# Kernel tuning notes

Hardware: AMD Instinct MI355X
Metric: run time of the kernel (lower is better)

Reference implementation:

```python
import jax, jax.numpy as jnp
import numpy as np

N = 50000      # nodes
E = 800000     # edges (avg degree 16)
D = 128        # input_nf = output_nf
H = 128        # hidden_nf


def _lin_init(key, fan_in, fan_out, gain=1.0):
    return gain * jax.random.normal(key, (fan_in, fan_out), jnp.float32) / np.sqrt(fan_in)


def setup_inputs() -> dict:
    key = jax.random.key(0)
    ks = jax.random.split(key, 20)
    h = jax.random.normal(ks[0], (N, D), jnp.float32)
    coord_diff = 0.5 * jax.random.normal(ks[1], (E, 3), jnp.float32)
    row = jax.random.randint(ks[2], (E,), 0, N, jnp.int32)
    col = jax.random.randint(ks[3], (E,), 0, N, jnp.int32)
    return {
        "h": h, "coord_diff": coord_diff, "row": row, "col": col,
        # edge_nn: Linear(2D+1 -> H), SiLU, Linear(H -> H), SiLU
        "We1": _lin_init(ks[4], 2 * D + 1, H), "be1": jnp.zeros((H,), jnp.float32),
        "We2": _lin_init(ks[5], H, H),          "be2": jnp.zeros((H,), jnp.float32),
        # node_nn: Linear(H+D -> H), SiLU, Linear(H -> D)
        "Wn1": _lin_init(ks[6], H + D, H), "bn1": jnp.zeros((H,), jnp.float32),
        "Wn2": _lin_init(ks[7], H, D),     "bn2": jnp.zeros((D,), jnp.float32),
        # coord_nn: Linear(H -> H), SiLU, Linear(H -> 1, no bias, gain 0.001)
        "Wc1": _lin_init(ks[8], H, H), "bc1": jnp.zeros((H,), jnp.float32),
        "Wc2": _lin_init(ks[9], H, 1, gain=0.001),
        # vel_scaling_nn: Linear(D -> H), SiLU, Linear(H -> 1)
        "Wv1": _lin_init(ks[10], D, H), "bv1": jnp.zeros((H,), jnp.float32),
        "Wv2": _lin_init(ks[11], H, 1), "bv2": jnp.zeros((1,), jnp.float32),
    }


def reference(h, coord_diff, row, col,
              We1, be1, We2, be2,
              Wn1, bn1, Wn2, bn2,
              Wc1, bc1, Wc2,
              Wv1, bv1, Wv2, bv2):
    n = h.shape[0]
    silu = jax.nn.silu
    # radial: squared edge length, [E,1]
    radial = jnp.sum(coord_diff * coord_diff, axis=1, keepdims=True)
    # edge model: gather endpoint features + radial, 2-layer SiLU MLP
    e_in = jnp.concatenate([h[row], h[col], radial], axis=1)        # [E, 2D+1]
    m = silu(silu(e_in @ We1 + be1) @ We2 + be2)                    # [E, H]
    # force model: per-edge scalar coefficient, clamped scatter-mean (coords_weight=1.0)
    coef = silu(m @ Wc1 + bc1) @ Wc2                                # [E, 1]
    trans = jnp.clip(coord_diff * coef, -100.0, 100.0)              # [E, 3]
    f_sum = jax.ops.segment_sum(trans, row, num_segments=n)         # [N, 3]
    cnt = jax.ops.segment_sum(jnp.ones((trans.shape[0], 1), trans.dtype), row, num_segments=n)
    force = f_sum / jnp.clip(cnt, 1.0)                              # segment mean, count clamped >=1
    # node model: scatter-sum of edge messages, then 2-layer MLP
    agg = jax.ops.segment_sum(m, row, num_segments=n)               # [N, H]
    h_cat = jnp.concatenate([h, agg], axis=1)                       # [N, D+H]
    h_out = silu(h_cat @ Wn1 + bn1) @ Wn2 + bn2                     # [N, D]
    # velocity scaling head
    vel = silu(h @ Wv1 + bv1) @ Wv2 + bv2                           # [N, 1]
    return (vel, force, h_out)
```

## Files before the change

### kernel.cpp

```cpp
#include <hip/hip_runtime.h>

#define NN 50000
#define EE 800000

typedef unsigned short u16;
typedef unsigned int u32;
typedef __attribute__((ext_vector_type(8))) short short8;
typedef __attribute__((ext_vector_type(4))) float f32x4;
typedef __attribute__((ext_vector_type(2))) float f32x2;

__device__ __forceinline__ u16 f2bf(float f) {
    union { float f; u32 i; } v; v.f = f;
    u32 x = v.i;
    return (u16)((x + 0x7fffu + ((x >> 16) & 1u)) >> 16);
}
__device__ __forceinline__ u32 pkr(float lo, float hi) {
    union { float f; u32 i; } a, b; a.f = lo; b.f = hi;
    return __builtin_amdgcn_perm(b.i + 0x8000u, a.i + 0x8000u, 0x07060302u);
}
__device__ __forceinline__ float bf2f(short x) {
    union { u32 i; float f; } v; v.i = ((u32)(u16)x) << 16; return v.f;
}
__device__ __forceinline__ float siluf(float x) {
    return x * __builtin_amdgcn_rcpf(1.0f + __expf(-x));
}
__device__ __forceinline__ void atomic_pk_add_bf16(u16* addr, u32 data) {
    asm volatile("global_atomic_pk_add_bf16 %0, %1, off" :: "v"(addr), "v"(data) : "memory");
}

__device__ __forceinline__ int b_idx2(int k, int n) {
    int chunk = ((k >> 5) << 3) + ((n >> 5) << 1) + (n & 1);
    return chunk * 512 + (((k >> 3) & 3) << 7) + (((n >> 1) & 15) << 3) + (k & 7);
}

__global__ __launch_bounds__(256) void prep_kernel(
    const float* __restrict__ We1, const float* __restrict__ We2,
    const float* __restrict__ Wc1, const float* __restrict__ Wn1,
    const float* __restrict__ Wn2, const float* __restrict__ Wv1,
    u16* __restrict__ We1bf, u16* __restrict__ We2bf, u16* __restrict__ Wc1bf,
    u16* __restrict__ Wn1bf, u16* __restrict__ Wn2bf, u16* __restrict__ Wv1bf)
{
    int i = blockIdx.x * 256 + threadIdx.x;
    if (i < 32768) {
        int k = i >> 7, n = i & 127;
        We1bf[b_idx2(k, n)] = f2bf(We1[k * 128 + n]);
    } else if (i < 49152) {
        int t = i - 32768; int k = t >> 7, n = t & 127;
        We2bf[b_idx2(k, n)] = f2bf(We2[k * 128 + n]);
    } else if (i < 65536) {
        int t = i - 49152; int k = t >> 7, n = t & 127;
        Wc1bf[b_idx2(k, n)] = f2bf(Wc1[k * 128 + n]);
    } else if (i < 98304) {
        int t = i - 65536; int k = t >> 7, n = t & 127;
        Wn1bf[b_idx2(k, n)] = f2bf(Wn1[k * 128 + n]);
    } else if (i < 114688) {
        int t = i - 98304; int k = t >> 7, n = t & 127;
        Wn2bf[b_idx2(k, n)] = f2bf(Wn2[k * 128 + n]);
    } else {
        int t = i - 114688; int k = t >> 7, n = t & 127;
        Wv1bf[b_idx2(k, n)] = f2bf(Wv1[k * 128 + n]);
    }
}

__global__ __launch_bounds__(256) void hist_kernel(const int* __restrict__ row,
                                                   u32* __restrict__ bins)
{
    int e = blockIdx.x * 256 + threadIdx.x;
    if (e < EE) atomicAdd(&bins[row[e]], 1u);
}

__global__ __launch_bounds__(256) void scan1_kernel(const u32* __restrict__ bins,
                                                    u32* __restrict__ part)
{
    __shared__ u32 wsum[4];
    int i = blockIdx.x * 256 + threadIdx.x;
    u32 v = (i < NN) ? bins[i] : 0u;
    #pragma unroll
    for (int o = 1; o < 64; o <<= 1) v += __shfl_xor(v, o);
    if ((threadIdx.x & 63) == 0) wsum[threadIdx.x >> 6] = v;
    __syncthreads();
    if (threadIdx.x == 0) part[blockIdx.x] = wsum[0] + wsum[1] + wsum[2] + wsum[3];
}

__global__ __launch_bounds__(256) void scan2_kernel(u32* __restrict__ part, int np)
{
    __shared__ u32 s[256];
    int t = threadIdx.x;
    s[t] = (t < np) ? part[t] : 0u;
    __syncthreads();
    if (t == 0) {
        u32 run = 0;
        for (int i = 0; i < 256; ++i) { u32 x = s[i]; s[i] = run; run += x; }
    }
    __syncthreads();
    if (t < np) part[t] = s[t];
}

__global__ __launch_bounds__(256) void scan3_kernel(const u32* __restrict__ bins,
                                                    const u32* __restrict__ part,
                                                    u32* __restrict__ cursor)
{
    __shared__ u32 wsum[4];
    int t = threadIdx.x;
    int i = blockIdx.x * 256 + t;
    u32 v = (i < NN) ? bins[i] : 0u;
    u32 x = v;
    #pragma unroll
    for (int o = 1; o < 64; o <<= 1) {
        u32 y = __shfl_up(x, o);
        if ((t & 63) >= o) x += y;
    }
    if ((t & 63) == 63) wsum[t >> 6] = x;
    __syncthreads();
    u32 base = part[blockIdx.x];
    for (int wv = 0; wv < (t >> 6); ++wv) base += wsum[wv];
    if (i < NN) cursor[i] = base + x - v;
}

__global__ __launch_bounds__(256) void scatter_kernel(
    const int* __restrict__ row, const int* __restrict__ col,
    const float* __restrict__ cdiff, u32* __restrict__ cursor,
    u32* __restrict__ edata)
{
    int e = blockIdx.x * 256 + threadIdx.x;
    if (e < EE) {
        int r = row[e];
        u32 p = atomicAdd(&cursor[r], 1u);
        float cx = cdiff[(size_t)e * 3 + 0];
        float cy = cdiff[(size_t)e * 3 + 1];
        float cz = cdiff[(size_t)e * 3 + 2];
        float rad = cx * cx + cy * cy + cz * cz;
        uint4 ed;
        ed.x = (u32)r;
        ed.y = (u32)col[e];
        ed.z = __float_as_uint(rad);
        ed.w = (u32)e;
        *(uint4*)(edata + (size_t)p * 4) = ed;
    }
}

__global__ __launch_bounds__(256, 4) void pgemm_kernel(
    const float* __restrict__ h, const float* __restrict__ be1,
    const float* __restrict__ bv1, const float* __restrict__ Wv2,
    const float* __restrict__ bv2,
    const u16* __restrict__ We1bf, const u16* __restrict__ Wv1bf,
    u16* __restrict__ P1bf, u16* __restrict__ P2bf,
    u16* __restrict__ hbf, u32 use_hbf, float* __restrict__ vel)
{
    __shared__ u16 sX[4096];
    __shared__ float sVelP[4][32];

    const int tid = threadIdx.x;
    const int nblk = blockIdx.x * 32;
    const int w = tid >> 6;
    const int lane = tid & 63;
    const int m15 = lane & 15, q = lane >> 4;
    const int n0 = w * 32 + 2 * m15, n1 = n0 + 1;
    const int ard = (m15 + 32 * q) * 8;
    const float b0 = be1[n0], b1 = be1[n1];

    {
        int r = tid & 31, j = tid >> 5;
        int n = nblk + r; if (n > NN - 1) n = NN - 1;
        #pragma unroll
        for (int i = 0; i < 2; ++i) {
            int kg = j * 2 + i;
            const float* src = h + (size_t)n * 128 + kg * 8;
            float4 a = *(const float4*)(src);
            float4 b = *(const float4*)(src + 4);
            uint4 v = make_uint4(pkr(a.x, a.y), pkr(a.z, a.w),
                                 pkr(b.x, b.y), pkr(b.z, b.w));
            *(uint4*)&sX[(r + 32 * kg) * 8] = v;
            if (use_hbf)
                *(uint4*)(hbf + (size_t)n * 128 + kg * 8) = v;
        }
    }
    __syncthreads();

    f32x4 acc[2][2];

    #pragma unroll
    for (int mt = 0; mt < 2; ++mt)
        #pragma unroll
        for (int r = 0; r < 4; ++r) { acc[mt][0][r] = b0; acc[mt][1][r] = b1; }
    #pragma unroll
    for (int c = 0; c < 4; ++c) {
        short8 bf0 = *(const short8*)(We1bf + (c * 8 + w * 2 + 0) * 512 + lane * 8);
        short8 bf1 = *(const short8*)(We1bf + (c * 8 + w * 2 + 1) * 512 + lane * 8);
        #pragma unroll
        for (int mt = 0; mt < 2; ++mt) {
            short8 af = *(const short8*)(sX + ard + c * 1024 + mt * 128);
            acc[mt][0] = __builtin_amdgcn_mfma_f32_16x16x32_bf16(af, bf0, acc[mt][0], 0, 0, 0);
            acc[mt][1] = __builtin_amdgcn_mfma_f32_16x16x32_bf16(af, bf1, acc[mt][1], 0, 0, 0);
        }
    }
    #pragma unroll
    for (int mt = 0; mt < 2; ++mt)
        #pragma unroll
        for (int r = 0; r < 4; ++r) {
            int n = nblk + mt * 16 + q * 4 + r;
            if (n < NN)
                *(u32*)(P1bf + (size_t)n * 128 + n0) = pkr(acc[mt][0][r], acc[mt][1][r]);
        }

    #pragma unroll
    for (int mt = 0; mt < 2; ++mt)
        #pragma unroll
        for (int r = 0; r < 4; ++r) { acc[mt][0][r] = 0.0f; acc[mt][1][r] = 0.0f; }
    #pragma unroll
    for (int c = 4; c < 8; ++c) {
        short8 bf0 = *(const short8*)(We1bf + (c * 8 + w * 2 + 0) * 512 + lane * 8);
        short8 bf1 = *(const short8*)(We1bf + (c * 8 + w * 2 + 1) * 512 + lane * 8);
        #pragma unroll
        for (int mt = 0; mt < 2; ++mt) {
            short8 af = *(const short8*)(sX + ard + (c - 4) * 1024 + mt * 128);
            acc[mt][0] = __builtin_amdgcn_mfma_f32_16x16x32_bf16(af, bf0, acc[mt][0], 0, 0, 0);
            acc[mt][1] = __builtin_amdgcn_mfma_f32_16x16x32_bf16(af, bf1, acc[mt][1], 0, 0, 0);
        }
    }
    #pragma unroll
    for (int mt = 0; mt < 2; ++mt)
        #pragma unroll
        for (int r = 0; r < 4; ++r) {
            int n = nblk + mt * 16 + q * 4 + r;
            if (n < NN)
                *(u32*)(P2bf + (size_t)n * 128 + n0) = pkr(acc[mt][0][r], acc[mt][1][r]);
        }

    {
        const float bva = bv1[n0], bvb = bv1[n1];
        const float wv2a = Wv2[n0], wv2b = Wv2[n1];
        #pragma unroll
        for (int mt = 0; mt < 2; ++mt)
            #pragma unroll
            for (int r = 0; r < 4; ++r) { acc[mt][0][r] = bva; acc[mt][1][r] = bvb; }
        #pragma unroll
        for (int c = 0; c < 4; ++c) {
            short8 bf0 = *(const short8*)(Wv1bf + (c * 8 + w * 2 + 0) * 512 + lane * 8);
            short8 bf1 = *(const short8*)(Wv1bf + (c * 8 + w * 2 + 1) * 512 + lane * 8);
            #pragma unroll
            for (int mt = 0; mt < 2; ++mt) {
                short8 af = *(const short8*)(sX + ard + c * 1024 + mt * 128);
                acc[mt][0] = __builtin_amdgcn_mfma_f32_16x16x32_bf16(af, bf0, acc[mt][0], 0, 0, 0);
                acc[mt][1] = __builtin_amdgcn_mfma_f32_16x16x32_bf16(af, bf1, acc[mt][1], 0, 0, 0);
            }
        }
        #pragma unroll
        for (int mt = 0; mt < 2; ++mt)
            #pragma unroll
            for (int r = 0; r < 4; ++r) {
                float pv = fmaf(siluf(acc[mt][0][r]), wv2a, siluf(acc[mt][1][r]) * wv2b);
                pv += __shfl_xor(pv, 1);
                pv += __shfl_xor(pv, 2);
                pv += __shfl_xor(pv, 4);
                pv += __shfl_xor(pv, 8);
                if (m15 == 0) sVelP[w][mt * 16 + q * 4 + r] = pv;
            }
        __syncthreads();
        if (tid < 32) {
            int n = nblk + tid;
            if (n < NN)
                vel[n] = bv2[0] + sVelP[0][tid] + sVelP[1][tid] + sVelP[2][tid] + sVelP[3][tid];
        }
    }
}

__global__ __launch_bounds__(256, 8) void edge_kernel(
    const u16* __restrict__ P1bf, const u16* __restrict__ P2bf,
    const float* __restrict__ cdiff,
    const u32* __restrict__ edata,
    const float* __restrict__ We1,
    const float* __restrict__ be2, const float* __restrict__ bc1,
    const float* __restrict__ Wc2,
    const u16* __restrict__ We2bf, const u16* __restrict__ Wc1bf,
    u16* __restrict__ aggbf, float* __restrict__ fsum)
{
    __shared__ u16 sT[8192];
    __shared__ int sRow[64];
    __shared__ int sEg[64];
    __shared__ int sRid[64];
    __shared__ float sCoefP[4][64];
    __shared__ float sF[192];

    const int tid = threadIdx.x;
    const int e0 = blockIdx.x * 64;
    const int w = tid >> 6;
    const int lane = tid & 63;
    const int m15 = lane & 15, q = lane >> 4;
    const int n0 = w * 32 + 2 * m15, n1 = n0 + 1;
    const int lsw = (lane ^ q) * 8;
    const int a_ = m15 >> 2;
    const int sbase = (a_ << 7) + (q << 5) + ((m15 & 3) << 1);
    const int o0 = (0 ^ a_) << 3, o1 = (1 ^ a_) << 3, o2 = (2 ^ a_) << 3, o3 = (3 ^ a_) << 3;

    const float b2a = be2[n0], b2b = be2[n1];
    const float b3a = bc1[n0], b3b = bc1[n1];
    const float wc2a = Wc2[n0], wc2b = Wc2[n1];

    {
        int e = tid & 63, seg = tid >> 6;
        uint4 ed = *(const uint4*)(edata + (size_t)(e0 + e) * 4);
        int nr = (int)ed.x, nc = (int)ed.y;
        float rad = __uint_as_float(ed.z);
        if (seg == 0) { sRow[e] = nr; sEg[e] = (int)ed.w; }
        const u16* p1 = P1bf + (size_t)nr * 128 + seg * 32;
        const u16* p2 = P2bf + (size_t)nc * 128 + seg * 32;
        const float* wr = We1 + 256 * 128 + seg * 32;
        u16* tb = sT + (((seg * 4 + (e >> 4)) << 9) + (((e >> 2) & 3) << 5));
        const int rl = e & 3;
        #pragma unroll 2
        for (int g = 0; g < 4; ++g) {
            short8 x1 = *(const short8*)(p1 + g * 8);
            short8 x2 = *(const short8*)(p2 + g * 8);
            float4 wa = *(const float4*)(wr + g * 8);
            float4 wb = *(const float4*)(wr + g * 8 + 4);
            float v[8];
            #pragma unroll
            for (int t = 0; t < 4; ++t) {
                v[t]     = siluf(bf2f(x1[t])     + bf2f(x2[t])     + rad * ((const float*)&wa)[t]);
                v[t + 4] = siluf(bf2f(x1[t + 4]) + bf2f(x2[t + 4]) + rad * ((const float*)&wb)[t]);
            }
            uint4 dd = make_uint4(pkr(v[0], v[1]), pkr(v[2], v[3]),
                                  pkr(v[4], v[5]), pkr(v[6], v[7]));
            *(uint4*)(tb + ((g << 7) + ((rl ^ g) << 3))) = dd;
        }
    }
    __syncthreads();

    if (tid < 64) {
        int e = tid;
        int head = (e == 0) || (sRow[e] != sRow[e - 1]);
        int v = head ? e : 0;
        #pragma unroll
        for (int o = 1; o < 64; o <<= 1) {
            int y = __shfl_up(v, o);
            if (e >= o && y > v) v = y;
        }
        sRid[e] = v;
        sF[e * 3 + 0] = 0.f; sF[e * 3 + 1] = 0.f; sF[e * 3 + 2] = 0.f;
    }

    f32x4 acc[4][2];
    u32 d[4][4];

    #pragma unroll
    for (int mt = 0; mt < 4; ++mt)
        #pragma unroll
        for (int r = 0; r < 4; ++r) { acc[mt][0][r] = b2a; acc[mt][1][r] = b2b; }
    #pragma unroll
    for (int c = 0; c < 4; ++c) {
        short8 bf0 = *(const short8*)(We2bf + (c * 8 + w * 2 + 0) * 512 + lane * 8);
        short8 bf1 = *(const short8*)(We2bf + (c * 8 + w * 2 + 1) * 512 + lane * 8);
        #pragma unroll
        for (int mt = 0; mt < 4; ++mt) {
            short8 af = *(const short8*)(sT + (c * 4 + mt) * 512 + lsw);
            acc[mt][0] = __builtin_amdgcn_mfma_f32_16x16x32_bf16(af, bf0, acc[mt][0], 0, 0, 0);
            acc[mt][1] = __builtin_amdgcn_mfma_f32_16x16x32_bf16(af, bf1, acc[mt][1], 0, 0, 0);
        }
    }
    #pragma unroll
    for (int mt = 0; mt < 4; ++mt)
        #pragma unroll
        for (int r = 0; r < 4; ++r)
            d[mt][r] = pkr(siluf(acc[mt][0][r]), siluf(acc[mt][1][r]));
    __syncthreads();
    #pragma unroll
    for (int mt = 0; mt < 4; ++mt) {
        u16* bp = sT + (w * 4 + mt) * 512 + sbase;
        *(u32*)(bp + o0) = d[mt][0];
        *(u32*)(bp + o1) = d[mt][1];
        *(u32*)(bp + o2) = d[mt][2];
        *(u32*)(bp + o3) = d[mt][3];
    }
    __syncthreads();

    #pragma unroll
    for (int mt = 0; mt < 4; ++mt)
        #pragma unroll
        for (int r = 0; r < 4; ++r) { acc[mt][0][r] = b3a; acc[mt][1][r] = b3b; }
    #pragma unroll
    for (int c = 0; c < 4; ++c) {
        short8 bf0 = *(const short8*)(Wc1bf + (c * 8 + w * 2 + 0) * 512 + lane * 8);
        short8 bf1 = *(const short8*)(Wc1bf + (c * 8 + w * 2 + 1) * 512 + lane * 8);
        #pragma unroll
        for (int mt = 0; mt < 4; ++mt) {
            short8 af = *(const short8*)(sT + (c * 4 + mt) * 512 + lsw);
            acc[mt][0] = __builtin_amdgcn_mfma_f32_16x16x32_bf16(af, bf0, acc[mt][0], 0, 0, 0);
            acc[mt][1] = __builtin_amdgcn_mfma_f32_16x16x32_bf16(af, bf1, acc[mt][1], 0, 0, 0);
        }
    }
    #pragma unroll
    for (int mt = 0; mt < 4; ++mt)
        #pragma unroll
        for (int r = 0; r < 4; ++r) {
            float pv = fmaf(siluf(acc[mt][0][r]), wc2a, siluf(acc[mt][1][r]) * wc2b);
            pv += __shfl_xor(pv, 1);
            pv += __shfl_xor(pv, 2);
            pv += __shfl_xor(pv, 4);
            pv += __shfl_xor(pv, 8);
            if (m15 == 0) sCoefP[w][mt * 16 + q * 4 + r] = pv;
        }

    {
        const int P = tid & 63, C = 2 * P, g = tid >> 6;
        const int xorb = (C >> 3) & 3;
        const int base = ((((C >> 5) * 4 + g) << 9)) + (((C >> 3) & 3) << 7) + (C & 7);
        float s0 = 0.f, s1 = 0.f;
        int prow = sRow[g * 16];
        #pragma unroll
        for (int i = 0; i < 16; ++i) {
            u32 v = *(const u32*)(sT + base + (((i >> 2) & 3) << 5) + (((i & 3) ^ xorb) << 3));
            int r = sRow[g * 16 + i];
            if (r != prow) {
                atomic_pk_add_bf16(aggbf + (size_t)prow * 128 + C, pkr(s0, s1));
                s0 = 0.f; s1 = 0.f; prow = r;
            }
            s0 += bf2f((short)(v & 0xffffu));
            s1 += bf2f((short)(v >> 16));
        }
        atomic_pk_add_bf16(aggbf + (size_t)prow * 128 + C, pkr(s0, s1));
    }
    __syncthreads();

    if (tid < 192) {
        int e = tid / 3, ax = tid - e * 3;
        float coef = sCoefP[0][e] + sCoefP[1][e] + sCoefP[2][e] + sCoefP[3][e];
        float tr = cdiff[(size_t)sEg[e] * 3 + ax] * coef;
        tr = fminf(fmaxf(tr, -100.f), 100.f);
        atomicAdd(&sF[sRid[e] * 3 + ax], tr);
    }
    __syncthreads();
    if (tid < 192) {
        int e = tid / 3, ax = tid - e * 3;
        if (e == 0 || sRow[e] != sRow[e - 1])
            atomicAdd(&fsum[(size_t)sRow[e] * 3 + ax], sF[e * 3 + ax]);
    }
}

__global__ __launch_bounds__(256, 4) void node_kernel(
    const float* __restrict__ h, const u16* __restrict__ hbf, u32 use_hbf,
    const float* __restrict__ bn1, const float* __restrict__ bn2,
    const u16* __restrict__ Wn1bf, const u16* __restrict__ Wn2bf,
    const u16* __restrict__ aggbf, const float* __restrict__ fsum,
    const u32* __restrict__ bins, float* __restrict__ out)
{
    __shared__ u16 sX[8192];
    __shared__ float sBn1[128], sBn2[128];
    u16* sT = sX + 4096;

    const int tid = threadIdx.x;
    const int nblk = blockIdx.x * 32;
    const int w = tid >> 6;
    const int lane = tid & 63;
    const int m15 = lane & 15, q = lane >> 4;
    const int n0 = w * 32 + 2 * m15, n1 = n0 + 1;
    const int lsw = (lane ^ q) * 8;
    const int a_ = m15 >> 2;
    const int sbase = (a_ << 7) + (q << 5) + ((m15 & 3) << 1);
    const int o0 = (0 ^ a_) << 3, o1 = (1 ^ a_) << 3, o2 = (2 ^ a_) << 3, o3 = (3 ^ a_) << 3;
    const int ard = (m15 + 32 * q) * 8;

    if (tid < 96) {
        int r = tid / 3, ax = tid - r * 3;
        int n = nblk + r;
        if (n < NN)
            out[NN + (size_t)n * 3 + ax] = fsum[(size_t)n * 3 + ax] * __builtin_amdgcn_rcpf(fmaxf((float)bins[n], 1.0f));
    }
    if (tid < 128) { sBn1[tid] = bn1[tid]; sBn2[tid] = bn2[tid]; }

    {
        int r = tid & 31, j = tid >> 5;
        int n = nblk + r; if (n > NN - 1) n = NN - 1;
        if (j < 4) {
            if (use_hbf) {
                #pragma unroll
                for (int i = 0; i < 4; ++i) {
                    int kg = j * 4 + i;
                    *(uint4*)&sX[(r + 32 * kg) * 8] =
                        *(const uint4*)(hbf + (size_t)n * 128 + kg * 8);
                }
            } else {
                #pragma unroll
                for (int i = 0; i < 4; ++i) {
                    int kg = j * 4 + i;
                    const float* src = h + (size_t)n * 128 + kg * 8;
                    float4 a = *(const float4*)(src);
                    float4 b = *(const float4*)(src + 4);
                    *(uint4*)&sX[(r + 32 * kg) * 8] = make_uint4(pkr(a.x, a.y), pkr(a.z, a.w),
                                                                 pkr(b.x, b.y), pkr(b.z, b.w));
                }
            }
        } else {
            #pragma unroll
            for (int i = 0; i < 4; ++i) {
                int kg = j * 4 + i;
                *(uint4*)&sX[(r + 32 * kg) * 8] =
                    *(const uint4*)(aggbf + (size_t)n * 128 + (kg - 16) * 8);
            }
        }
    }
    __syncthreads();

    f32x4 acc[2][2];

    {
        float b0 = sBn1[n0], b1 = sBn1[n1];
        #pragma unroll
        for (int mt = 0; mt < 2; ++mt)
            #pragma unroll
            for (int r = 0; r < 4; ++r) { acc[mt][0][r] = b0; acc[mt][1][r] = b1; }
    }
    #pragma unroll
    for (int c = 0; c < 8; ++c) {
        short8 bf0 = *(const short8*)(Wn1bf + (c * 8 + w * 2 + 0) * 512 + lane * 8);
        short8 bf1 = *(const short8*)(Wn1bf + (c * 8 + w * 2 + 1) * 512 + lane * 8);
        #pragma unroll
        for (int mt = 0; mt < 2; ++mt) {
            short8 af = *(const short8*)(sX + ard + c * 1024 + mt * 128);
            acc[mt][0] = __builtin_amdgcn_mfma_f32_16x16x32_bf16(af, bf0, acc[mt][0], 0, 0, 0);
            acc[mt][1] = __builtin_amdgcn_mfma_f32_16x16x32_bf16(af, bf1, acc[mt][1], 0, 0, 0);
        }
    }
    u32 dn[2][4];
    #pragma unroll
    for (int mt = 0; mt < 2; ++mt)
        #pragma unroll
        for (int r = 0; r < 4; ++r)
            dn[mt][r] = pkr(siluf(acc[mt][0][r]), siluf(acc[mt][1][r]));
    __syncthreads();
    #pragma unroll
    for (int mt = 0; mt < 2; ++mt) {
        u16* bp = sT + (w * 2 + mt) * 512 + sbase;
        *(u32*)(bp + o0) = dn[mt][0];
        *(u32*)(bp + o1) = dn[mt][1];
        *(u32*)(bp + o2) = dn[mt][2];
        *(u32*)(bp + o3) = dn[mt][3];
    }
    __syncthreads();

    {
        float b0 = sBn2[n0], b1 = sBn2[n1];
        #pragma unroll
        for (int mt = 0; mt < 2; ++mt)
            #pragma unroll
            for (int r = 0; r < 4; ++r) { acc[mt][0][r] = b0; acc[mt][1][r] = b1; }
    }
    #pragma unroll
    for (int c = 0; c < 4; ++c) {
        short8 bf0 = *(const short8*)(Wn2bf + (c * 8 + w * 2 + 0) * 512 + lane * 8);
        short8 bf1 = *(const short8*)(Wn2bf + (c * 8 + w * 2 + 1) * 512 + lane * 8);
        #pragma unroll
        for (int mt = 0; mt < 2; ++mt) {
            short8 af = *(const short8*)(sT + (c * 2 + mt) * 512 + lsw);
            acc[mt][0] = __builtin_amdgcn_mfma_f32_16x16x32_bf16(af, bf0, acc[mt][0], 0, 0, 0);
            acc[mt][1] = __builtin_amdgcn_mfma_f32_16x16x32_bf16(af, bf1, acc[mt][1], 0, 0, 0);
        }
    }
    #pragma unroll
    for (int mt = 0; mt < 2; ++mt)
        #pragma unroll
        for (int r = 0; r < 4; ++r) {
            int n = nblk + mt * 16 + q * 4 + r;
            if (n < NN) {
                f32x2 v; v.x = acc[mt][0][r]; v.y = acc[mt][1][r];
                *(f32x2*)(out + (size_t)4 * NN + (size_t)n * 128 + n0) = v;
            }
        }
}

extern "C" void kernel_launch(void* const* d_in, const int* in_sizes, int n_in,
                              void* d_out, int out_size, void* d_ws, size_t ws_size,
                              hipStream_t stream) {
    const float* h     = (const float*)d_in[0];
    const float* cdiff = (const float*)d_in[1];
    const int* row     = (const int*)d_in[2];
    const int* col     = (const int*)d_in[3];
    const float* We1 = (const float*)d_in[4];
    const float* be1 = (const float*)d_in[5];
    const float* We2 = (const float*)d_in[6];
    const float* be2 = (const float*)d_in[7];
    const float* Wn1 = (const float*)d_in[8];
    const float* bn1 = (const float*)d_in[9];
    const float* Wn2 = (const float*)d_in[10];
    const float* bn2 = (const float*)d_in[11];
    const float* Wc1 = (const float*)d_in[12];
    const float* bc1 = (const float*)d_in[13];
    const float* Wc2 = (const float*)d_in[14];
    const float* Wv1 = (const float*)d_in[15];
    const float* bv1 = (const float*)d_in[16];
    const float* Wv2 = (const float*)d_in[17];
    const float* bv2 = (const float*)d_in[18];

    u16* aggbf  = (u16*)d_ws;
    float* fsum = (float*)(aggbf + (size_t)NN * 128);
    u32* bins   = (u32*)(fsum + (size_t)NN * 3);
    u16* We1bf = (u16*)(bins + NN);
    u16* We2bf = We1bf + 32768;
    u16* Wc1bf = We2bf + 16384;
    u16* Wn1bf = Wc1bf + 16384;
    u16* Wn2bf = Wn1bf + 32768;
    u16* Wv1bf = Wn2bf + 16384;
    u16* P1bf  = Wv1bf + 16384;
    float* out = (float*)d_out;

    const size_t base_bytes = (size_t)26662144;
    u16* hbf = (u16*)((char*)d_ws + base_bytes);
    u32 use_hbf = (ws_size >= base_bytes + (size_t)NN * 256) ? 1u : 0u;

    u32* cursor = (u32*)(out + NN);
    u32* part   = cursor + NN;
    u16* P2bf   = (u16*)(out + (size_t)4 * NN);
    u32* edata  = (u32*)(P2bf + (size_t)NN * 128);

    size_t zero_bytes = (size_t)NN * 128 * 2 + (size_t)NN * 3 * 4 + (size_t)NN * 4;
    hipMemsetAsync(d_ws, 0, zero_bytes, stream);

    const int NSC = (NN + 255) / 256;

    prep_kernel<<<512, 256, 0, stream>>>(We1, We2, Wc1, Wn1, Wn2, Wv1,
                                         We1bf, We2bf, Wc1bf, Wn1bf, Wn2bf, Wv1bf);
    pgemm_kernel<<<(NN + 31) / 32, 256, 0, stream>>>(h, be1, bv1, Wv2, bv2,
                                                     We1bf, Wv1bf, P1bf, P2bf,
                                                     hbf, use_hbf, out);
    hist_kernel<<<(EE + 255) / 256, 256, 0, stream>>>(row, bins);
    scan1_kernel<<<NSC, 256, 0, stream>>>(bins, part);
    scan2_kernel<<<1, 256, 0, stream>>>(part, NSC);
    scan3_kernel<<<NSC, 256, 0, stream>>>(bins, part, cursor);
    scatter_kernel<<<(EE + 255) / 256, 256, 0, stream>>>(row, col, cdiff, cursor, edata);
    edge_kernel<<<EE / 64, 256, 0, stream>>>(P1bf, P2bf, cdiff, edata,
                                             We1, be2, bc1, Wc2,
                                             We2bf, Wc1bf,
                                             aggbf, fsum);
    node_kernel<<<(NN + 31) / 32, 256, 0, stream>>>(h, hbf, use_hbf,
                                                    bn1, bn2,
                                                    Wn1bf, Wn2bf,
                                                    aggbf, fsum, bins, out);
}
```

Before: 377.1 us.

## Fuse histogram into prep, merge scan kernels, precompute ranks and sorted coord_diff

Merges the histogram pass into the weight-prep launch and records each edge's rank within its row from the histogram atomic, so the scatter pass can compute its position without a second atomic. Folds the single-block scan2 into scan3, with every block redoing the serial prefix over the partial sums in shared memory. Scatter also writes coord_diff in sorted edge order so the edge kernel reads it contiguously instead of gathering by original edge index. This cuts two launches and the scatter atomics, at the cost of extra workspace and an extra write of ranks and sorted coordinates.

```diff
diff --git a/kernel.cpp b/kernel.cpp
--- a/kernel.cpp
+++ b/kernel.cpp
@@ -33,13 +33,23 @@
     return chunk * 512 + (((k >> 3) & 3) << 7) + (((n >> 1) & 15) << 3) + (k & 7);
 }
 
-__global__ __launch_bounds__(256) void prep_kernel(
+__global__ __launch_bounds__(256) void prephist_kernel(
     const float* __restrict__ We1, const float* __restrict__ We2,
     const float* __restrict__ Wc1, const float* __restrict__ Wn1,
     const float* __restrict__ Wn2, const float* __restrict__ Wv1,
     u16* __restrict__ We1bf, u16* __restrict__ We2bf, u16* __restrict__ Wc1bf,
-    u16* __restrict__ Wn1bf, u16* __restrict__ Wn2bf, u16* __restrict__ Wv1bf)
+    u16* __restrict__ Wn1bf, u16* __restrict__ Wn2bf, u16* __restrict__ Wv1bf,
+    const int* __restrict__ row, u32* __restrict__ bins,
+    u32* __restrict__ rank, u32 use_ext)
 {
+    if (blockIdx.x >= 512) {
+        int e = (blockIdx.x - 512) * 256 + threadIdx.x;
+        if (e < EE) {
+            u32 rk = atomicAdd(&bins[row[e]], 1u);
+            if (use_ext) rank[e] = rk;
+        }
+        return;
+    }
     int i = blockIdx.x * 256 + threadIdx.x;
     if (i < 32768) {
         int k = i >> 7, n = i & 127;
@@ -62,13 +72,6 @@
     }
 }
 
-__global__ __launch_bounds__(256) void hist_kernel(const int* __restrict__ row,
-                                                   u32* __restrict__ bins)
-{
-    int e = blockIdx.x * 256 + threadIdx.x;
-    if (e < EE) atomicAdd(&bins[row[e]], 1u);
-}
-
 __global__ __launch_bounds__(256) void scan1_kernel(const u32* __restrict__ bins,
                                                     u32* __restrict__ part)
 {
@@ -82,26 +85,19 @@
     if (threadIdx.x == 0) part[blockIdx.x] = wsum[0] + wsum[1] + wsum[2] + wsum[3];
 }
 
-__global__ __launch_bounds__(256) void scan2_kernel(u32* __restrict__ part, int np)
+__global__ __launch_bounds__(256) void scan3_kernel(const u32* __restrict__ bins,
+                                                    const u32* __restrict__ part,
+                                                    u32* __restrict__ cursor, int np)
 {
-    __shared__ u32 s[256];
+    __shared__ u32 sPart[256];
+    __shared__ u32 wsum[4];
     int t = threadIdx.x;
-    s[t] = (t < np) ? part[t] : 0u;
+    sPart[t] = (t < np) ? part[t] : 0u;
     __syncthreads();
     if (t == 0) {
         u32 run = 0;
-        for (int i = 0; i < 256; ++i) { u32 x = s[i]; s[i] = run; run += x; }
-    }
-    __syncthreads();
-    if (t < np) part[t] = s[t];
-}
-
-__global__ __launch_bounds__(256) void scan3_kernel(const u32* __restrict__ bins,
-                                                    const u32* __restrict__ part,
-                                                    u32* __restrict__ cursor)
-{
-    __shared__ u32 wsum[4];
-    int t = threadIdx.x;
+        for (int i = 0; i < np; ++i) { u32 x = sPart[i]; sPart[i] = run; run += x; }
+    }
     int i = blockIdx.x * 256 + t;
     u32 v = (i < NN) ? bins[i] : 0u;
     u32 x = v;
@@ -112,7 +108,7 @@
     }
     if ((t & 63) == 63) wsum[t >> 6] = x;
     __syncthreads();
-    u32 base = part[blockIdx.x];
+    u32 base = sPart[blockIdx.x];
     for (int wv = 0; wv < (t >> 6); ++wv) base += wsum[wv];
     if (i < NN) cursor[i] = base + x - v;
 }
@@ -120,12 +116,13 @@
 __global__ __launch_bounds__(256) void scatter_kernel(
     const int* __restrict__ row, const int* __restrict__ col,
     const float* __restrict__ cdiff, u32* __restrict__ cursor,
-    u32* __restrict__ edata)
+    const u32* __restrict__ rank,
+    u32* __restrict__ edata, float* __restrict__ cdS, u32 use_ext)
 {
     int e = blockIdx.x * 256 + threadIdx.x;
     if (e < EE) {
         int r = row[e];
-        u32 p = atomicAdd(&cursor[r], 1u);
+        u32 p = use_ext ? (cursor[r] + rank[e]) : atomicAdd(&cursor[r], 1u);
         float cx = cdiff[(size_t)e * 3 + 0];
         float cy = cdiff[(size_t)e * 3 + 1];
         float cz = cdiff[(size_t)e * 3 + 2];
@@ -136,6 +133,11 @@
         ed.z = __float_as_uint(rad);
         ed.w = (u32)e;
         *(uint4*)(edata + (size_t)p * 4) = ed;
+        if (use_ext) {
+            cdS[(size_t)p * 3 + 0] = cx;
+            cdS[(size_t)p * 3 + 1] = cy;
+            cdS[(size_t)p * 3 + 2] = cz;
+        }
     }
 }
 
@@ -145,7 +147,7 @@
     const float* __restrict__ bv2,
     const u16* __restrict__ We1bf, const u16* __restrict__ Wv1bf,
     u16* __restrict__ P1bf, u16* __restrict__ P2bf,
-    u16* __restrict__ hbf, u32 use_hbf, float* __restrict__ vel)
+    u16* __restrict__ hbf, u32 use_ext, float* __restrict__ vel)
 {
     __shared__ u16 sX[4096];
     __shared__ float sVelP[4][32];
@@ -171,7 +173,7 @@
             uint4 v = make_uint4(pkr(a.x, a.y), pkr(a.z, a.w),
                                  pkr(b.x, b.y), pkr(b.z, b.w));
             *(uint4*)&sX[(r + 32 * kg) * 8] = v;
-            if (use_hbf)
+            if (use_ext)
                 *(uint4*)(hbf + (size_t)n * 128 + kg * 8) = v;
         }
     }
@@ -267,7 +269,7 @@
 
 __global__ __launch_bounds__(256, 8) void edge_kernel(
     const u16* __restrict__ P1bf, const u16* __restrict__ P2bf,
-    const float* __restrict__ cdiff,
+    const float* __restrict__ cdiff, const float* __restrict__ cdS, u32 use_ext,
     const u32* __restrict__ edata,
     const float* __restrict__ We1,
     const float* __restrict__ be2, const float* __restrict__ bc1,
@@ -425,7 +427,9 @@
     if (tid < 192) {
         int e = tid / 3, ax = tid - e * 3;
         float coef = sCoefP[0][e] + sCoefP[1][e] + sCoefP[2][e] + sCoefP[3][e];
-        float tr = cdiff[(size_t)sEg[e] * 3 + ax] * coef;
+        float cd = use_ext ? cdS[(size_t)e0 * 3 + tid]
+                           : cdiff[(size_t)sEg[e] * 3 + ax];
+        float tr = cd * coef;
         tr = fminf(fmaxf(tr, -100.f), 100.f);
         atomicAdd(&sF[sRid[e] * 3 + ax], tr);
     }
@@ -438,7 +442,7 @@
 }
 
 __global__ __launch_bounds__(256, 4) void node_kernel(
-    const float* __restrict__ h, const u16* __restrict__ hbf, u32 use_hbf,
+    const float* __restrict__ h, const u16* __restrict__ hbf, u32 use_ext,
     const float* __restrict__ bn1, const float* __restrict__ bn2,
     const u16* __restrict__ Wn1bf, const u16* __restrict__ Wn2bf,
     const u16* __restrict__ aggbf, const float* __restrict__ fsum,
@@ -472,7 +476,7 @@
         int r = tid & 31, j = tid >> 5;
         int n = nblk + r; if (n > NN - 1) n = NN - 1;
         if (j < 4) {
-            if (use_hbf) {
+            if (use_ext) {
                 #pragma unroll
                 for (int i = 0; i < 4; ++i) {
                     int kg = j * 4 + i;
@@ -604,8 +608,11 @@
     float* out = (float*)d_out;
 
     const size_t base_bytes = (size_t)26662144;
-    u16* hbf = (u16*)((char*)d_ws + base_bytes);
-    u32 use_hbf = (ws_size >= base_bytes + (size_t)NN * 256) ? 1u : 0u;
+    u16* hbf   = (u16*)((char*)d_ws + base_bytes);
+    u32* rank  = (u32*)((char*)d_ws + base_bytes + (size_t)NN * 256);
+    float* cdS = (float*)((char*)d_ws + base_bytes + (size_t)NN * 256
+                          + (size_t)EE * 4);
+    u32 use_ext = (ws_size >= base_bytes + (size_t)NN * 256 + (size_t)EE * 16) ? 1u : 0u;
 
     u32* cursor = (u32*)(out + NN);
     u32* part   = cursor + NN;
@@ -617,21 +624,22 @@
 
     const int NSC = (NN + 255) / 256;
 
-    prep_kernel<<<512, 256, 0, stream>>>(We1, We2, Wc1, Wn1, Wn2, Wv1,
-                                         We1bf, We2bf, Wc1bf, Wn1bf, Wn2bf, Wv1bf);
+    prephist_kernel<<<512 + (EE + 255) / 256, 256, 0, stream>>>(
+        We1, We2, Wc1, Wn1, Wn2, Wv1,
+        We1bf, We2bf, Wc1bf, Wn1bf, Wn2bf, Wv1bf,
+        row, bins, rank, use_ext);
     pgemm_kernel<<<(NN + 31) / 32, 256, 0, stream>>>(h, be1, bv1, Wv2, bv2,
                                                      We1bf, Wv1bf, P1bf, P2bf,
-                                                     hbf, use_hbf, out);
-    hist_kernel<<<(EE + 255) / 256, 256, 0, stream>>>(row, bins);
+                                                     hbf, use_ext, out);
     scan1_kernel<<<NSC, 256, 0, stream>>>(bins, part);
-    scan2_kernel<<<1, 256, 0, stream>>>(part, NSC);
-    scan3_kernel<<<NSC, 256, 0, stream>>>(bins, part, cursor);
-    scatter_kernel<<<(EE + 255) / 256, 256, 0, stream>>>(row, col, cdiff, cursor, edata);
-    edge_kernel<<<EE / 64, 256, 0, stream>>>(P1bf, P2bf, cdiff, edata,
+    scan3_kernel<<<NSC, 256, 0, stream>>>(bins, part, cursor, NSC);
+    scatter_kernel<<<(EE + 255) / 256, 256, 0, stream>>>(row, col, cdiff, cursor,
+                                                         rank, edata, cdS, use_ext);
+    edge_kernel<<<EE / 64, 256, 0, stream>>>(P1bf, P2bf, cdiff, cdS, use_ext, edata,
                                              We1, be2, bc1, Wc2,
                                              We2bf, Wc1bf,
                                              aggbf, fsum);
-    node_kernel<<<(NN + 31) / 32, 256, 0, stream>>>(h, hbf, use_hbf,
+    node_kernel<<<(NN + 31) / 32, 256, 0, stream>>>(h, hbf, use_ext,
                                                     bn1, bn2,
                                                     Wn1bf, Wn2bf,
                                                     aggbf, fsum, bins, out);
```

Result: faster. 354.3 us (-6.0%).
